# Kernel optimization log

Hardware: AMD Instinct MI355X
Metric: run time of the kernel (lower is better)

Reference implementation:

```python
import jax, jax.numpy as jnp
import numpy as np
import math

H = 5       # attention heads
DK = 20     # attdim // H
ATT = 100   # attdim
LAYERS = 2
B, L, BERT_DIM = 32, 256, 768


def _layernorm(x, a, b, eps=1e-6):
    mean = x.mean(-1, keepdims=True)
    std = jnp.std(x, axis=-1, ddof=1, keepdims=True)  # torch.std is unbiased
    return a * (x - mean) / (std + eps) + b


def _forward(sequence_output, src_mask, aspect_mask, short_mask,
             ln_a, ln_b, Wxx_w, Wxx_b, q_w, q_b, k_w, k_b,
             dense_w, dense_b, bias_m, W_w, W_b, Wx_w, Wx_b, clf_w, clf_b):
    Bn, Ln, _ = sequence_output.shape
    x = _layernorm(sequence_output, ln_a, ln_b)
    g = x @ Wxx_w + Wxx_b                                  # [B,L,100]
    asp_wn = aspect_mask.sum(1, keepdims=True)             # [B,1]
    aspect = (g * aspect_mask[..., None]).sum(1) / asp_wn  # [B,100]

    q = (g @ q_w + q_b).reshape(Bn, Ln, H, DK).transpose(0, 2, 1, 3)  # [B,H,L,dk]
    k = (g @ k_w + k_b).reshape(Bn, Ln, H, DK).transpose(0, 2, 1, 3)
    # aspect is expanded identically across heads/positions before dense -> [B,dk]
    asp = aspect @ dense_w + dense_b                       # [B,dk]
    scores = jnp.einsum('bhid,bhjd->bhij', q, k) / math.sqrt(DK)
    asp_sc = jnp.tanh(jnp.einsum('bd,bhjd->bhj', asp, k) + bias_m[0])
    scores = scores + asp_sc[:, :, None, :]
    scores = jnp.where(src_mask[:, None, None, :] == 0, -1e9, scores)
    scores = scores + short_mask                           # [B,1,L,L] broadcast
    adj = jax.nn.softmax(scores, axis=-1)                  # [B,H,L,L]

    # edge-update linear split so the [B,L,L,205] concat is never materialized:
    # edge[b,i,j] = adj_perm[b,i,j] @ Wa + go[b,j] @ W1 + go[b,i] @ W2 + b
    Wa, W1, W2 = Wx_w[:H], Wx_w[H:H + ATT], Wx_w[H + ATT:]
    go = g
    for i in range(LAYERS):
        # expand+matmul+mean over heads == mean-head message passing
        Ax = jnp.einsum('bhij,bjd->bid', adj, go) / H
        go = jax.nn.relu(Ax @ W_w + W_b)
        if i < LAYERS - 1:  # last edge update is discarded by the original output
            edge = (jnp.einsum('bhij,hk->bijk', adj, Wa)
                    + (go @ W1)[:, None, :, :]
                    + (go @ W2)[:, :, None, :]
                    + Wx_b)
            adj = edge.transpose(0, 3, 1, 2)
    # original: node_outputs = F.relu(gcn_outputs) (aggregate_W result is overwritten)
    h = jax.nn.relu(go)
    out1 = (h * aspect_mask[..., None]).sum(1) / asp_wn    # [B,100]
    return out1 @ clf_w + clf_b                            # [B,3]


def setup_inputs() -> dict:
    key = jax.random.key(0)
    ks = jax.random.split(key, 24)
    f32 = jnp.float32
    p = lambda k, shape, s=0.05: jax.random.normal(k, shape, dtype=f32) * s
    src_mask = jax.random.randint(ks[0], (B, L), 0, 2, dtype=jnp.int32).at[:, 0].set(1)
    aspect_mask = jnp.zeros((B, L), f32).at[:, 4:8].set(1.0)  # aspect span tokens
    return {
        'sequence_output': jax.random.normal(ks[1], (B, L, BERT_DIM), dtype=f32),
        'src_mask': src_mask,
        'aspect_mask': aspect_mask,
        'short_mask': p(ks[2], (B, 1, L, L), 1.0),
        'ln_a': jnp.ones((BERT_DIM,), f32),
        'ln_b': jnp.zeros((BERT_DIM,), f32),
        'Wxx_w': p(ks[3], (BERT_DIM, ATT)), 'Wxx_b': p(ks[4], (ATT,)),
        'q_w': p(ks[5], (ATT, ATT)), 'q_b': p(ks[6], (ATT,)),
        'k_w': p(ks[7], (ATT, ATT)), 'k_b': p(ks[8], (ATT,)),
        'dense_w': p(ks[9], (ATT, DK)), 'dense_b': p(ks[10], (DK,)),
        'bias_m': p(ks[11], (1,)),
        'W_w': p(ks[12], (ATT, ATT)), 'W_b': p(ks[13], (ATT,)),
        'Wx_w': p(ks[14], (H + 2 * ATT, H)), 'Wx_b': p(ks[15], (H,)),
        'clf_w': p(ks[16], (ATT, 3)), 'clf_b': p(ks[17], (3,)),
    }


def reference(sequence_output, src_mask, aspect_mask, short_mask,
              ln_a, ln_b, Wxx_w, Wxx_b, q_w, q_b, k_w, k_b,
              dense_w, dense_b, bias_m, W_w, W_b, Wx_w, Wx_b, clf_w, clf_b):
    return _forward(sequence_output, src_mask, aspect_mask, short_mask,
                    ln_a, ln_b, Wxx_w, Wxx_b, q_w, q_b, k_w, k_b,
                    dense_w, dense_b, bias_m, W_w, W_b, Wx_w, Wx_b, clf_w, clf_b)
```

## Files before the change

kernel.cpp:

```cpp
#include <hip/hip_runtime.h>
#include <math.h>

constexpr int CL = 256;
constexpr int CD = 768;
constexpr int CATT = 100;
constexpr int CH = 5;
constexpr int CDK = 20;

__device__ __forceinline__ void fma4(float4& a, float s, const float4& w) {
    a.x = fmaf(s, w.x, a.x);
    a.y = fmaf(s, w.y, a.y);
    a.z = fmaf(s, w.z, a.z);
    a.w = fmaf(s, w.w, a.w);
}

__global__ __launch_bounds__(256, 3) void k1_fused(
    const float* __restrict__ x, const float* __restrict__ ln_a,
    const float* __restrict__ ln_b, const float* __restrict__ Wxx_w,
    const float* __restrict__ Wxx_b, const float* __restrict__ q_w,
    const float* __restrict__ q_b, const float* __restrict__ k_w,
    const float* __restrict__ k_b, const float* __restrict__ amask,
    float* __restrict__ g, float* __restrict__ qt, float* __restrict__ ktb,
    float* __restrict__ aspect_raw)
{
    __shared__ float s_w[2][3200];
    __shared__ float s_xn[2][16 * 36];
    __shared__ float s_gt[16 * 100];
    __shared__ float s_ln[1536];
    __shared__ float s_mean[16], s_rinv[16];

    const int t = threadIdx.x;
    const int r0 = blockIdx.x * 16;
    const int wid = t >> 6, lane = t & 63;

    if (t < 192) {
        ((float4*)s_ln)[t] = ((const float4*)ln_a)[t];
        ((float4*)(s_ln + 768))[t] = ((const float4*)ln_b)[t];
    }

    for (int rr = wid * 4; rr < wid * 4 + 4; ++rr) {
        const float* xr = x + (size_t)(r0 + rr) * CD;
        float xv[12];
        float s = 0.f;
#pragma unroll
        for (int m = 0; m < 12; ++m) { xv[m] = xr[lane + 64 * m]; s += xv[m]; }
#pragma unroll
        for (int o = 32; o; o >>= 1) s += __shfl_xor(s, o);
        float mean = s * (1.0f / 768.0f);
        float sq = 0.f;
#pragma unroll
        for (int m = 0; m < 12; ++m) { float d = xv[m] - mean; sq = fmaf(d, d, sq); }
#pragma unroll
        for (int o = 32; o; o >>= 1) sq += __shfl_xor(sq, o);
        if (lane == 0) {
            s_mean[rr] = mean;
            s_rinv[rr] = 1.0f / (sqrtf(sq * (1.0f / 767.0f)) + 1e-6f);
        }
    }

    const float4* wsrc = (const float4*)Wxx_w;
    float4 w0 = wsrc[t], w1 = wsrc[t + 256], w2 = wsrc[t + 512], w3;
    if (t < 32) w3 = wsrc[t + 768];
    const int rA = t >> 5, cA = t & 31;
    float xa = x[(size_t)(r0 + rA) * CD + cA];
    float xb = x[(size_t)(r0 + rA + 8) * CD + cA];

    __syncthreads();

    {
        float4* d4 = (float4*)s_w[0];
        d4[t] = w0; d4[t + 256] = w1; d4[t + 512] = w2;
        if (t < 32) d4[t + 768] = w3;
        float la = s_ln[cA], lbv = s_ln[768 + cA];
        s_xn[0][rA * 36 + cA] = fmaf(la, (xa - s_mean[rA]) * s_rinv[rA], lbv);
        s_xn[0][(rA + 8) * 36 + cA] = fmaf(la, (xb - s_mean[rA + 8]) * s_rinv[rA + 8], lbv);
    }
    __syncthreads();

    const int cg = t % 25, rg = t / 25;
    const int c = cg * 4;
    float4 acc0 = make_float4(0.f, 0.f, 0.f, 0.f);
    float4 acc1 = make_float4(0.f, 0.f, 0.f, 0.f);

    for (int kt = 0; kt < 24; ++kt) {
        if (kt < 23) {
            const float4* ws = wsrc + (size_t)(kt + 1) * 800;
            w0 = ws[t]; w1 = ws[t + 256]; w2 = ws[t + 512];
            if (t < 32) w3 = ws[t + 768];
            int gc = (kt + 1) * 32 + cA;
            xa = x[(size_t)(r0 + rA) * CD + gc];
            xb = x[(size_t)(r0 + rA + 8) * CD + gc];
        }
        if (t < 200) {
            const float* wb = s_w[kt & 1];
            const float* xbuf = s_xn[kt & 1];
#pragma unroll 2
            for (int kk = 0; kk < 32; kk += 4) {
                float4 a0 = *(const float4*)&xbuf[(rg * 2 + 0) * 36 + kk];
                float4 a1 = *(const float4*)&xbuf[(rg * 2 + 1) * 36 + kk];
                float4 v0 = *(const float4*)&wb[(kk + 0) * 100 + c];
                float4 v1 = *(const float4*)&wb[(kk + 1) * 100 + c];
                float4 v2 = *(const float4*)&wb[(kk + 2) * 100 + c];
                float4 v3 = *(const float4*)&wb[(kk + 3) * 100 + c];
                fma4(acc0, a0.x, v0); fma4(acc0, a0.y, v1); fma4(acc0, a0.z, v2); fma4(acc0, a0.w, v3);
                fma4(acc1, a1.x, v0); fma4(acc1, a1.y, v1); fma4(acc1, a1.z, v2); fma4(acc1, a1.w, v3);
            }
        }
        if (kt < 23) {
            float4* d4 = (float4*)s_w[(kt + 1) & 1];
            d4[t] = w0; d4[t + 256] = w1; d4[t + 512] = w2;
            if (t < 32) d4[t + 768] = w3;
            int gc = (kt + 1) * 32 + cA;
            float la = s_ln[gc], lbv = s_ln[768 + gc];
            float* xd = s_xn[(kt + 1) & 1];
            xd[rA * 36 + cA] = fmaf(la, (xa - s_mean[rA]) * s_rinv[rA], lbv);
            xd[(rA + 8) * 36 + cA] = fmaf(la, (xb - s_mean[rA + 8]) * s_rinv[rA + 8], lbv);
        }
        __syncthreads();
    }

    if (t < 200) {
        float4 bias = *(const float4*)&Wxx_b[c];
        float4 rv0, rv1;
        rv0.x = acc0.x + bias.x; rv0.y = acc0.y + bias.y; rv0.z = acc0.z + bias.z; rv0.w = acc0.w + bias.w;
        rv1.x = acc1.x + bias.x; rv1.y = acc1.y + bias.y; rv1.z = acc1.z + bias.z; rv1.w = acc1.w + bias.w;
        float4 rv[2] = { rv0, rv1 };
#pragma unroll
        for (int q = 0; q < 2; ++q) {
            int row = r0 + rg * 2 + q;
            *(float4*)&g[(size_t)row * CATT + c] = rv[q];
            *(float4*)&s_gt[(rg * 2 + q) * 100 + c] = rv[q];
            float m = amask[row];
            if (m != 0.f) {
                int b = row >> 8;
                atomicAdd(&aspect_raw[b * CATT + c + 0], m * rv[q].x);
                atomicAdd(&aspect_raw[b * CATT + c + 1], m * rv[q].y);
                atomicAdd(&aspect_raw[b * CATT + c + 2], m * rv[q].z);
                atomicAdd(&aspect_raw[b * CATT + c + 3], m * rv[q].w);
            }
        }
    }

    const float4* qw4 = (const float4*)q_w;
    const float4* kw4 = (const float4*)k_w;
    float4 sA = qw4[t], sB;
    if (t < 244) sB = qw4[t + 256];
    __syncthreads();
    {
        float4* d4 = (float4*)s_w[0];
        d4[t] = sA; if (t < 244) d4[t + 256] = sB;
    }
    __syncthreads();

    float4 p0 = make_float4(0.f, 0.f, 0.f, 0.f);
    float4 p1 = make_float4(0.f, 0.f, 0.f, 0.f);
    for (int tau = 0; tau < 10; ++tau) {
        if (tau < 9) {
            const float4* src = (tau + 1 < 5) ? qw4 + (size_t)(tau + 1) * 500
                                              : kw4 + (size_t)(tau - 4) * 500;
            sA = src[t]; if (t < 244) sB = src[t + 256];
        }
        if (t < 200) {
            const float* wb = s_w[tau & 1];
            const int kb = (tau % 5) * 20;
#pragma unroll 2
            for (int kk = 0; kk < 20; kk += 4) {
                float4 a0 = *(const float4*)&s_gt[(rg * 2 + 0) * 100 + kb + kk];
                float4 a1 = *(const float4*)&s_gt[(rg * 2 + 1) * 100 + kb + kk];
                float4 v0 = *(const float4*)&wb[(kk + 0) * 100 + c];
                float4 v1 = *(const float4*)&wb[(kk + 1) * 100 + c];
                float4 v2 = *(const float4*)&wb[(kk + 2) * 100 + c];
                float4 v3 = *(const float4*)&wb[(kk + 3) * 100 + c];
                fma4(p0, a0.x, v0); fma4(p0, a0.y, v1); fma4(p0, a0.z, v2); fma4(p0, a0.w, v3);
                fma4(p1, a1.x, v0); fma4(p1, a1.y, v1); fma4(p1, a1.z, v2); fma4(p1, a1.w, v3);
            }
            if (tau == 4 || tau == 9) {
                const float* bb = (tau == 4) ? q_b : k_b;
                float* outp = (tau == 4) ? qt : ktb;
                float4 bias = *(const float4*)&bb[c];
                p0.x += bias.x; p0.y += bias.y; p0.z += bias.z; p0.w += bias.w;
                p1.x += bias.x; p1.y += bias.y; p1.z += bias.z; p1.w += bias.w;
                const int h = c / CDK, d = c % CDK;
                float4 rv[2] = { p0, p1 };
#pragma unroll
                for (int q = 0; q < 2; ++q) {
                    int row = r0 + rg * 2 + q;
                    int bidx = row >> 8, l = row & 255;
                    *(float4*)&outp[((size_t)(bidx * CH + h) * CL + l) * CDK + d] = rv[q];
                }
                p0 = make_float4(0.f, 0.f, 0.f, 0.f);
                p1 = make_float4(0.f, 0.f, 0.f, 0.f);
            }
        }
        if (tau < 9) {
            float4* d4 = (float4*)s_w[(tau + 1) & 1];
            d4[t] = sA; if (t < 244) d4[t + 256] = sB;
        }
        __syncthreads();
    }
}

__global__ __launch_bounds__(256, 3) void k45_attn_gcn0(
    const float* __restrict__ qt, const float* __restrict__ ktb,
    const float* __restrict__ aspect_raw, const float* __restrict__ amask,
    const float* __restrict__ dense_w, const float* __restrict__ dense_b,
    const float* __restrict__ bias_m, const int* __restrict__ src_mask,
    const float* __restrict__ shortm, const float* __restrict__ Wx_w,
    const float* __restrict__ g, const float* __restrict__ W_w,
    const float* __restrict__ W_b, float* __restrict__ adjW,
    float* __restrict__ go1, float* __restrict__ t1, float* __restrict__ t2,
    float* __restrict__ gW2S)
{
    constexpr int ICH = 16;
    __shared__ float s_pool[16 * 260];
    __shared__ float s_w[2][3200];
    __shared__ float s_q[CH * 320];
    __shared__ float s_red[CH][64];
    __shared__ float s_was[5];
    __shared__ float s_aspb[20];
    __shared__ float s_w1[100], s_w2[100];
    __shared__ float s_g1row[16];

    const int b = blockIdx.x >> 4, ic = blockIdx.x & 15;
    const int i0 = ic * ICH;
    const int t = threadIdx.x, lane = t & 63, wid = t >> 6;
    const int j = t;

    if (t < 5) {
        float s = 0.f;
        for (int k2 = 0; k2 < 5; ++k2) s += Wx_w[t * 5 + k2];
        s_was[t] = s;
    }
    if (t < 100) {
        float a = 0.f, c2 = 0.f;
#pragma unroll
        for (int h = 0; h < 5; ++h) {
            a += Wx_w[(5 + t) * 5 + h];
            c2 += Wx_w[(105 + t) * 5 + h];
        }
        s_w1[t] = a; s_w2[t] = c2;
    }
    float wn = 0.f;
    if (t < 64) {
        float4 mv = ((const float4*)amask)[b * 64 + t];
        wn = mv.x + mv.y + mv.z + mv.w;
#pragma unroll
        for (int o = 32; o; o >>= 1) wn += __shfl_xor(wn, o);
    }
    if (t < 20) {
        float a = 0.f;
        for (int d = 0; d < CATT; ++d)
            a = fmaf(aspect_raw[b * CATT + d], dense_w[d * CDK + t], a);
        s_aspb[t] = a / wn + dense_b[t];
    }
    {
        const float* qbase = qt + (size_t)b * CH * CL * CDK + (size_t)i0 * CDK;
        for (int i = t; i < CH * 320; i += 256) {
            int h = i / 320, r = i % 320;
            s_q[i] = qbase[(size_t)h * CL * CDK + r];
        }
    }

    const bool masked = (src_mask[b * CL + j] == 0);
    const float bm = bias_m[0];
    const float rs20 = 0.223606797749978969f;

    float sm[ICH];
#pragma unroll
    for (int ii = 0; ii < ICH; ++ii)
        sm[ii] = shortm[(size_t)(b * CL + i0 + ii) * CL + j];

    float accS[ICH], accW[ICH];
#pragma unroll
    for (int ii = 0; ii < ICH; ++ii) { accS[ii] = 0.f; accW[ii] = 0.f; }

    __syncthreads();

    for (int h = 0; h < CH; ++h) {
        float4 kr[5];
        const float* kp = ktb + ((size_t)(b * CH + h) * CL + j) * CDK;
#pragma unroll
        for (int m = 0; m < 5; ++m) kr[m] = *(const float4*)(kp + 4 * m);
        const float was_h = s_was[h];
        float s = bm;
#pragma unroll
        for (int m = 0; m < 5; ++m) {
            s = fmaf(s_aspb[4 * m + 0], kr[m].x, s);
            s = fmaf(s_aspb[4 * m + 1], kr[m].y, s);
            s = fmaf(s_aspb[4 * m + 2], kr[m].z, s);
            s = fmaf(s_aspb[4 * m + 3], kr[m].w, s);
        }
        const float aspsc = tanhf(s);

        float pv[ICH];
#pragma unroll
        for (int ii = 0; ii < ICH; ++ii) {
            const float* qrow = &s_q[h * 320 + ii * CDK];
            float sc = 0.f;
#pragma unroll
            for (int m = 0; m < 5; ++m) {
                float4 q4 = *(const float4*)(qrow + 4 * m);
                sc = fmaf(q4.x, kr[m].x, sc);
                sc = fmaf(q4.y, kr[m].y, sc);
                sc = fmaf(q4.z, kr[m].z, sc);
                sc = fmaf(q4.w, kr[m].w, sc);
            }
            sc = fmaf(sc, rs20, aspsc) + sm[ii];
            float p = masked ? 0.f : __expf(sc);
            pv[ii] = p;
            float ssum = p;
#pragma unroll
            for (int o = 32; o; o >>= 1) ssum += __shfl_xor(ssum, o);
            if (lane == 0) s_red[h][ii * 4 + wid] = ssum;
        }
        __syncthreads();
#pragma unroll
        for (int ii = 0; ii < ICH; ++ii) {
            float tot = s_red[h][ii * 4 + 0] + s_red[h][ii * 4 + 1] +
                        s_red[h][ii * 4 + 2] + s_red[h][ii * 4 + 3];
            float pn = pv[ii] * __frcp_rn(tot);
            accS[ii] += pn;
            accW[ii] = fmaf(was_h, pn, accW[ii]);
        }
    }

#pragma unroll
    for (int ii = 0; ii < ICH; ++ii) {
        adjW[(size_t)(b * CL + i0 + ii) * CL + j] = accW[ii];
        s_pool[ii * 260 + j] = accS[ii];
    }

    const int cg = t % 25, rg = t / 25;
    const int c = cg * 4;
    const float4* g4 = (const float4*)g + (size_t)b * 6400;
    float4 sA = g4[t], sB = g4[t + 256], sC = g4[t + 512], sD;
    if (t < 32) sD = g4[t + 768];
    {
        float4* d4 = (float4*)s_w[0];
        d4[t] = sA; d4[t + 256] = sB; d4[t + 512] = sC;
        if (t < 32) d4[t + 768] = sD;
    }
    __syncthreads();

    float4 acc0 = make_float4(0.f, 0.f, 0.f, 0.f);
    float4 acc1 = make_float4(0.f, 0.f, 0.f, 0.f);
    for (int jt = 0; jt < 8; ++jt) {
        if (jt < 7) {
            const float4* src = g4 + (size_t)(jt + 1) * 800;
            sA = src[t]; sB = src[t + 256]; sC = src[t + 512];
            if (t < 32) sD = src[t + 768];
        }
        if (t < 200) {
            const float* wb = s_w[jt & 1];
#pragma unroll 2
            for (int kk = 0; kk < 32; kk += 4) {
                float4 a0 = *(const float4*)&s_pool[(rg * 2 + 0) * 260 + jt * 32 + kk];
                float4 a1 = *(const float4*)&s_pool[(rg * 2 + 1) * 260 + jt * 32 + kk];
                float4 v0 = *(const float4*)&wb[(kk + 0) * 100 + c];
                float4 v1 = *(const float4*)&wb[(kk + 1) * 100 + c];
                float4 v2 = *(const float4*)&wb[(kk + 2) * 100 + c];
                float4 v3 = *(const float4*)&wb[(kk + 3) * 100 + c];
                fma4(acc0, a0.x, v0); fma4(acc0, a0.y, v1); fma4(acc0, a0.z, v2); fma4(acc0, a0.w, v3);
                fma4(acc1, a1.x, v0); fma4(acc1, a1.y, v1); fma4(acc1, a1.z, v2); fma4(acc1, a1.w, v3);
            }
        }
        if (jt < 7) {
            float4* d4 = (float4*)s_w[(jt + 1) & 1];
            d4[t] = sA; d4[t + 256] = sB; d4[t + 512] = sC;
            if (t < 32) d4[t + 768] = sD;
        }
        __syncthreads();
    }

    float* s_ax = s_pool;
    if (t < 200) {
        float4 r;
        r.x = acc0.x * 0.2f; r.y = acc0.y * 0.2f; r.z = acc0.z * 0.2f; r.w = acc0.w * 0.2f;
        *(float4*)&s_ax[(rg * 2 + 0) * 108 + c] = r;
        r.x = acc1.x * 0.2f; r.y = acc1.y * 0.2f; r.z = acc1.z * 0.2f; r.w = acc1.w * 0.2f;
        *(float4*)&s_ax[(rg * 2 + 1) * 108 + c] = r;
    }
    const float4* ww4 = (const float4*)W_w;
    sA = ww4[t]; if (t < 244) sB = ww4[t + 256];
    {
        float4* d4 = (float4*)s_w[0];
        d4[t] = sA; if (t < 244) d4[t + 256] = sB;
    }
    __syncthreads();

    float4 o0 = make_float4(0.f, 0.f, 0.f, 0.f);
    float4 o1 = make_float4(0.f, 0.f, 0.f, 0.f);
    for (int wt = 0; wt < 5; ++wt) {
        if (wt < 4) {
            const float4* src = ww4 + (size_t)(wt + 1) * 500;
            sA = src[t]; if (t < 244) sB = src[t + 256];
        }
        if (t < 200) {
            const float* wb = s_w[wt & 1];
            const int kb = wt * 20;
#pragma unroll 2
            for (int kk = 0; kk < 20; kk += 4) {
                float4 a0 = *(const float4*)&s_ax[(rg * 2 + 0) * 108 + kb + kk];
                float4 a1 = *(const float4*)&s_ax[(rg * 2 + 1) * 108 + kb + kk];
                float4 v0 = *(const float4*)&wb[(kk + 0) * 100 + c];
                float4 v1 = *(const float4*)&wb[(kk + 1) * 100 + c];
                float4 v2 = *(const float4*)&wb[(kk + 2) * 100 + c];
                float4 v3 = *(const float4*)&wb[(kk + 3) * 100 + c];
                fma4(o0, a0.x, v0); fma4(o0, a0.y, v1); fma4(o0, a0.z, v2); fma4(o0, a0.w, v3);
                fma4(o1, a1.x, v0); fma4(o1, a1.y, v1); fma4(o1, a1.z, v2); fma4(o1, a1.w, v3);
            }
        }
        if (wt < 4) {
            float4* d4 = (float4*)s_w[(wt + 1) & 1];
            d4[t] = sA; if (t < 244) d4[t + 256] = sB;
        }
        __syncthreads();
    }

    float* s_go = s_pool + 1728;
    if (t < 200) {
        float4 bias = *(const float4*)&W_b[c];
        o0.x = fmaxf(o0.x + bias.x, 0.f); o0.y = fmaxf(o0.y + bias.y, 0.f);
        o0.z = fmaxf(o0.z + bias.z, 0.f); o0.w = fmaxf(o0.w + bias.w, 0.f);
        o1.x = fmaxf(o1.x + bias.x, 0.f); o1.y = fmaxf(o1.y + bias.y, 0.f);
        o1.z = fmaxf(o1.z + bias.z, 0.f); o1.w = fmaxf(o1.w + bias.w, 0.f);
        *(float4*)&go1[(size_t)(b * CL + i0 + rg * 2 + 0) * CATT + c] = o0;
        *(float4*)&go1[(size_t)(b * CL + i0 + rg * 2 + 1) * CATT + c] = o1;
        *(float4*)&s_go[(rg * 2 + 0) * 104 + c] = o0;
        *(float4*)&s_go[(rg * 2 + 1) * 104 + c] = o1;
    }
    __syncthreads();

    if (t < 128) {
        int r = t >> 3, seg = t & 7;
        int e0 = seg * 13, e1 = e0 + 13 < 100 ? e0 + 13 : 100;
        float a = 0.f, c2 = 0.f;
        for (int e = e0; e < e1; ++e) {
            float v = s_go[r * 104 + e];
            a = fmaf(v, s_w1[e], a);
            c2 = fmaf(v, s_w2[e], c2);
        }
        a += __shfl_xor(a, 1); a += __shfl_xor(a, 2); a += __shfl_xor(a, 4);
        c2 += __shfl_xor(c2, 1); c2 += __shfl_xor(c2, 2); c2 += __shfl_xor(c2, 4);
        if (seg == 0) {
            s_g1row[r] = a;
            gW2S[b * CL + i0 + r] = c2;
        }
    }
    __syncthreads();

    if (t < 100) {
        float a = 0.f, s2 = 0.f;
#pragma unroll
        for (int r = 0; r < 16; ++r) {
            float v = s_go[r * 104 + t];
            a = fmaf(s_g1row[r], v, a);
            s2 += v;
        }
        atomicAdd(&t1[b * CATT + t], a);
        atomicAdd(&t2[b * CATT + t], s2);
    }
}

__global__ __launch_bounds__(256, 3) void k7_gcn1(
    const float* __restrict__ adjW, const float* __restrict__ go1,
    const float* __restrict__ W_w, const float* __restrict__ W_b,
    const float* __restrict__ t1, const float* __restrict__ t2,
    const float* __restrict__ gW2S, const float* __restrict__ Wx_b,
    const float* __restrict__ amask, float* __restrict__ out1_raw)
{
    __shared__ float s_pool[16 * 260];
    __shared__ float s_w[2][3200];
    const int b = blockIdx.x >> 4, ic = blockIdx.x & 15;
    const int i0 = ic * 16;
    const int t = threadIdx.x;

    {
        const float4* asrc = (const float4*)adjW + (size_t)(b * CL + i0) * 64;
#pragma unroll
        for (int m = 0; m < 4; ++m) {
            int i = t + 256 * m;
            int row = i >> 6, c4 = i & 63;
            *(float4*)&s_pool[row * 260 + c4 * 4] = asrc[i];
        }
    }
    const int cg = t % 25, rg = t / 25;
    const int c = cg * 4;
    const float4* g4 = (const float4*)go1 + (size_t)b * 6400;
    float4 sA = g4[t], sB = g4[t + 256], sC = g4[t + 512], sD;
    if (t < 32) sD = g4[t + 768];
    {
        float4* d4 = (float4*)s_w[0];
        d4[t] = sA; d4[t + 256] = sB; d4[t + 512] = sC;
        if (t < 32) d4[t + 768] = sD;
    }
    __syncthreads();

    float4 acc0 = make_float4(0.f, 0.f, 0.f, 0.f);
    float4 acc1 = make_float4(0.f, 0.f, 0.f, 0.f);
    for (int jt = 0; jt < 8; ++jt) {
        if (jt < 7) {
            const float4* src = g4 + (size_t)(jt + 1) * 800;
            sA = src[t]; sB = src[t + 256]; sC = src[t + 512];
            if (t < 32) sD = src[t + 768];
        }
        if (t < 200) {
            const float* wb = s_w[jt & 1];
#pragma unroll 2
            for (int kk = 0; kk < 32; kk += 4) {
                float4 a0 = *(const float4*)&s_pool[(rg * 2 + 0) * 260 + jt * 32 + kk];
                float4 a1 = *(const float4*)&s_pool[(rg * 2 + 1) * 260 + jt * 32 + kk];
                float4 v0 = *(const float4*)&wb[(kk + 0) * 100 + c];
                float4 v1 = *(const float4*)&wb[(kk + 1) * 100 + c];
                float4 v2 = *(const float4*)&wb[(kk + 2) * 100 + c];
                float4 v3 = *(const float4*)&wb[(kk + 3) * 100 + c];
                fma4(acc0, a0.x, v0); fma4(acc0, a0.y, v1); fma4(acc0, a0.z, v2); fma4(acc0, a0.w, v3);
                fma4(acc1, a1.x, v0); fma4(acc1, a1.y, v1); fma4(acc1, a1.z, v2); fma4(acc1, a1.w, v3);
            }
        }
        if (jt < 7) {
            float4* d4 = (float4*)s_w[(jt + 1) & 1];
            d4[t] = sA; d4[t + 256] = sB; d4[t + 512] = sC;
            if (t < 32) d4[t + 768] = sD;
        }
        __syncthreads();
    }

    float* s_ax = s_pool;
    if (t < 200) {
        float wxbs = Wx_b[0] + Wx_b[1] + Wx_b[2] + Wx_b[3] + Wx_b[4];
        float4 t1v = *(const float4*)&t1[b * CATT + c];
        float4 t2v = *(const float4*)&t2[b * CATT + c];
        float gw0 = gW2S[b * CL + i0 + rg * 2 + 0] + wxbs;
        float gw1 = gW2S[b * CL + i0 + rg * 2 + 1] + wxbs;
        float4 r;
        r.x = (acc0.x + t1v.x + gw0 * t2v.x) * 0.2f;
        r.y = (acc0.y + t1v.y + gw0 * t2v.y) * 0.2f;
        r.z = (acc0.z + t1v.z + gw0 * t2v.z) * 0.2f;
        r.w = (acc0.w + t1v.w + gw0 * t2v.w) * 0.2f;
        *(float4*)&s_ax[(rg * 2 + 0) * 108 + c] = r;
        r.x = (acc1.x + t1v.x + gw1 * t2v.x) * 0.2f;
        r.y = (acc1.y + t1v.y + gw1 * t2v.y) * 0.2f;
        r.z = (acc1.z + t1v.z + gw1 * t2v.z) * 0.2f;
        r.w = (acc1.w + t1v.w + gw1 * t2v.w) * 0.2f;
        *(float4*)&s_ax[(rg * 2 + 1) * 108 + c] = r;
    }
    const float4* ww4 = (const float4*)W_w;
    sA = ww4[t]; if (t < 244) sB = ww4[t + 256];
    {
        float4* d4 = (float4*)s_w[0];
        d4[t] = sA; if (t < 244) d4[t + 256] = sB;
    }
    __syncthreads();

    float4 o0 = make_float4(0.f, 0.f, 0.f, 0.f);
    float4 o1 = make_float4(0.f, 0.f, 0.f, 0.f);
    for (int wt = 0; wt < 5; ++wt) {
        if (wt < 4) {
            const float4* src = ww4 + (size_t)(wt + 1) * 500;
            sA = src[t]; if (t < 244) sB = src[t + 256];
        }
        if (t < 200) {
            const float* wb = s_w[wt & 1];
            const int kb = wt * 20;
#pragma unroll 2
            for (int kk = 0; kk < 20; kk += 4) {
                float4 a0 = *(const float4*)&s_ax[(rg * 2 + 0) * 108 + kb + kk];
                float4 a1 = *(const float4*)&s_ax[(rg * 2 + 1) * 108 + kb + kk];
                float4 v0 = *(const float4*)&wb[(kk + 0) * 100 + c];
                float4 v1 = *(const float4*)&wb[(kk + 1) * 100 + c];
                float4 v2 = *(const float4*)&wb[(kk + 2) * 100 + c];
                float4 v3 = *(const float4*)&wb[(kk + 3) * 100 + c];
                fma4(o0, a0.x, v0); fma4(o0, a0.y, v1); fma4(o0, a0.z, v2); fma4(o0, a0.w, v3);
                fma4(o1, a1.x, v0); fma4(o1, a1.y, v1); fma4(o1, a1.z, v2); fma4(o1, a1.w, v3);
            }
        }
        if (wt < 4) {
            float4* d4 = (float4*)s_w[(wt + 1) & 1];
            d4[t] = sA; if (t < 244) d4[t + 256] = sB;
        }
        __syncthreads();
    }

    if (t < 200) {
        float4 bias = *(const float4*)&W_b[c];
        o0.x = fmaxf(o0.x + bias.x, 0.f); o0.y = fmaxf(o0.y + bias.y, 0.f);
        o0.z = fmaxf(o0.z + bias.z, 0.f); o0.w = fmaxf(o0.w + bias.w, 0.f);
        o1.x = fmaxf(o1.x + bias.x, 0.f); o1.y = fmaxf(o1.y + bias.y, 0.f);
        o1.z = fmaxf(o1.z + bias.z, 0.f); o1.w = fmaxf(o1.w + bias.w, 0.f);
        float4 ov[2] = { o0, o1 };
#pragma unroll
        for (int q = 0; q < 2; ++q) {
            int row = b * CL + i0 + rg * 2 + q;
            float m = amask[row];
            if (m != 0.f) {
                atomicAdd(&out1_raw[b * CATT + c + 0], m * ov[q].x);
                atomicAdd(&out1_raw[b * CATT + c + 1], m * ov[q].y);
                atomicAdd(&out1_raw[b * CATT + c + 2], m * ov[q].z);
                atomicAdd(&out1_raw[b * CATT + c + 3], m * ov[q].w);
            }
        }
    }
}

__global__ __launch_bounds__(64) void k8_small(
    const float* __restrict__ out1_raw, const float* __restrict__ amask,
    const float* __restrict__ clf_w, const float* __restrict__ clf_b,
    float* __restrict__ out)
{
    const int b = blockIdx.x, t = threadIdx.x;
    float4 mv = ((const float4*)amask)[b * 64 + t];
    float wn = mv.x + mv.y + mv.z + mv.w;
#pragma unroll
    for (int o = 32; o; o >>= 1) wn += __shfl_xor(wn, o);
    if (t < 3) {
        float rwn = 1.f / wn;
        float a = clf_b[t];
        for (int d = 0; d < CATT; ++d)
            a = fmaf(out1_raw[b * CATT + d] * rwn, clf_w[d * 3 + t], a);
        out[b * 3 + t] = a;
    }
}

extern "C" void kernel_launch(void* const* d_in, const int* in_sizes, int n_in,
                              void* d_out, int out_size, void* d_ws, size_t ws_size,
                              hipStream_t stream) {
    const float* seq     = (const float*)d_in[0];
    const int*   srcm    = (const int*)d_in[1];
    const float* amask   = (const float*)d_in[2];
    const float* shortm  = (const float*)d_in[3];
    const float* ln_a    = (const float*)d_in[4];
    const float* ln_b    = (const float*)d_in[5];
    const float* Wxx_w   = (const float*)d_in[6];
    const float* Wxx_b   = (const float*)d_in[7];
    const float* q_w     = (const float*)d_in[8];
    const float* q_b     = (const float*)d_in[9];
    const float* k_w     = (const float*)d_in[10];
    const float* k_b     = (const float*)d_in[11];
    const float* dense_w = (const float*)d_in[12];
    const float* dense_b = (const float*)d_in[13];
    const float* bias_m  = (const float*)d_in[14];
    const float* W_w     = (const float*)d_in[15];
    const float* W_b     = (const float*)d_in[16];
    const float* Wx_w    = (const float*)d_in[17];
    const float* Wx_b    = (const float*)d_in[18];
    const float* clf_w   = (const float*)d_in[19];
    const float* clf_b   = (const float*)d_in[20];
    float* out = (float*)d_out;

    float* ws         = (float*)d_ws;
    float* g          = ws;
    float* qt         = g + 819200;
    float* ktb        = qt + 819200;
    float* go1        = ktb + 819200;
    float* adjW       = go1 + 819200;
    float* aspect_raw = adjW + 2097152;
    float* t1         = aspect_raw + 3200;
    float* t2         = t1 + 3200;
    float* out1_raw   = t2 + 3200;
    float* gW2S       = out1_raw + 3200;

    hipMemsetAsync(aspect_raw, 0, 4 * 3200 * sizeof(float), stream);
    hipLaunchKernelGGL(k1_fused, dim3(512), dim3(256), 0, stream, seq, ln_a, ln_b,
                       Wxx_w, Wxx_b, q_w, q_b, k_w, k_b, amask, g, qt, ktb, aspect_raw);
    hipLaunchKernelGGL(k45_attn_gcn0, dim3(512), dim3(256), 0, stream,
                       qt, ktb, aspect_raw, amask, dense_w, dense_b, bias_m, srcm,
                       shortm, Wx_w, g, W_w, W_b, adjW, go1, t1, t2, gW2S);
    hipLaunchKernelGGL(k7_gcn1, dim3(512), dim3(256), 0, stream,
                       adjW, go1, W_w, W_b, t1, t2, gW2S, Wx_b, amask, out1_raw);
    hipLaunchKernelGGL(k8_small, dim3(32), dim3(64), 0, stream,
                       out1_raw, amask, clf_w, clf_b, out);
}
```

Before: 241.8 us.

## Fuse all stages into one cooperative persistent kernel with grid syncs

Merges the three main kernels and the classifier into a single cooperative kernel that uses grid-wide syncs between phases, with a fallback to separate launches if cooperative launch is unavailable. Each block keeps its adjW tile in shared memory across the phase boundary, so the global adjW write and re-read are dropped. This removes launch gaps and adjW traffic. In exchange, the larger shared-memory struct lowers occupancy to 2 blocks per CU, grid syncs add barrier cost, and an occupancy query runs on the host at every launch.

```diff
diff --git a/kernel.cpp b/kernel.cpp
--- a/kernel.cpp
+++ b/kernel.cpp
@@ -1,5 +1,8 @@
 #include <hip/hip_runtime.h>
+#include <hip/hip_cooperative_groups.h>
 #include <math.h>
+
+namespace cg = cooperative_groups;
 
 constexpr int CL = 256;
 constexpr int CD = 768;
@@ -14,7 +17,19 @@
     a.w = fmaf(s, w.w, a.w);
 }
 
-__global__ __launch_bounds__(256, 3) void k1_fused(
+struct SMem {
+    float w[2][3200];
+    float adjW[4160];
+    float pool[4160];
+    float q[1600];
+    float red[5][64];
+    float was[5], aspb[20];
+    float w1[100], w2[100], g1row[16];
+    float mean[16], rinv[16];
+};
+
+__device__ __forceinline__ void phase0(
+    SMem& sm, int blk, int t,
     const float* __restrict__ x, const float* __restrict__ ln_a,
     const float* __restrict__ ln_b, const float* __restrict__ Wxx_w,
     const float* __restrict__ Wxx_b, const float* __restrict__ q_w,
@@ -23,21 +38,17 @@
     float* __restrict__ g, float* __restrict__ qt, float* __restrict__ ktb,
     float* __restrict__ aspect_raw)
 {
-    __shared__ float s_w[2][3200];
-    __shared__ float s_xn[2][16 * 36];
-    __shared__ float s_gt[16 * 100];
-    __shared__ float s_ln[1536];
-    __shared__ float s_mean[16], s_rinv[16];
-
-    const int t = threadIdx.x;
-    const int r0 = blockIdx.x * 16;
+    const int r0 = blk * 16;
     const int wid = t >> 6, lane = t & 63;
+    float* s_gt = sm.pool;
+    float* s_ln = sm.pool + 1600;
+    float* s_xn0 = sm.q;
+    float* s_xn1 = sm.q + 576;
 
     if (t < 192) {
         ((float4*)s_ln)[t] = ((const float4*)ln_a)[t];
         ((float4*)(s_ln + 768))[t] = ((const float4*)ln_b)[t];
     }
-
     for (int rr = wid * 4; rr < wid * 4 + 4; ++rr) {
         const float* xr = x + (size_t)(r0 + rr) * CD;
         float xv[12];
@@ -53,8 +64,8 @@
 #pragma unroll
         for (int o = 32; o; o >>= 1) sq += __shfl_xor(sq, o);
         if (lane == 0) {
-            s_mean[rr] = mean;
-            s_rinv[rr] = 1.0f / (sqrtf(sq * (1.0f / 767.0f)) + 1e-6f);
+            sm.mean[rr] = mean;
+            sm.rinv[rr] = 1.0f / (sqrtf(sq * (1.0f / 767.0f)) + 1e-6f);
         }
     }
 
@@ -68,17 +79,17 @@
     __syncthreads();
 
     {
-        float4* d4 = (float4*)s_w[0];
+        float4* d4 = (float4*)sm.w[0];
         d4[t] = w0; d4[t + 256] = w1; d4[t + 512] = w2;
         if (t < 32) d4[t + 768] = w3;
         float la = s_ln[cA], lbv = s_ln[768 + cA];
-        s_xn[0][rA * 36 + cA] = fmaf(la, (xa - s_mean[rA]) * s_rinv[rA], lbv);
-        s_xn[0][(rA + 8) * 36 + cA] = fmaf(la, (xb - s_mean[rA + 8]) * s_rinv[rA + 8], lbv);
-    }
-    __syncthreads();
-
-    const int cg = t % 25, rg = t / 25;
-    const int c = cg * 4;
+        s_xn0[rA * 36 + cA] = fmaf(la, (xa - sm.mean[rA]) * sm.rinv[rA], lbv);
+        s_xn0[(rA + 8) * 36 + cA] = fmaf(la, (xb - sm.mean[rA + 8]) * sm.rinv[rA + 8], lbv);
+    }
+    __syncthreads();
+
+    const int cg2 = t % 25, rg = t / 25;
+    const int c = cg2 * 4;
     float4 acc0 = make_float4(0.f, 0.f, 0.f, 0.f);
     float4 acc1 = make_float4(0.f, 0.f, 0.f, 0.f);
 
@@ -92,8 +103,8 @@
             xb = x[(size_t)(r0 + rA + 8) * CD + gc];
         }
         if (t < 200) {
-            const float* wb = s_w[kt & 1];
-            const float* xbuf = s_xn[kt & 1];
+            const float* wb = sm.w[kt & 1];
+            const float* xbuf = (kt & 1) ? s_xn1 : s_xn0;
 #pragma unroll 2
             for (int kk = 0; kk < 32; kk += 4) {
                 float4 a0 = *(const float4*)&xbuf[(rg * 2 + 0) * 36 + kk];
@@ -107,14 +118,14 @@
             }
         }
         if (kt < 23) {
-            float4* d4 = (float4*)s_w[(kt + 1) & 1];
+            float4* d4 = (float4*)sm.w[(kt + 1) & 1];
             d4[t] = w0; d4[t + 256] = w1; d4[t + 512] = w2;
             if (t < 32) d4[t + 768] = w3;
             int gc = (kt + 1) * 32 + cA;
             float la = s_ln[gc], lbv = s_ln[768 + gc];
-            float* xd = s_xn[(kt + 1) & 1];
-            xd[rA * 36 + cA] = fmaf(la, (xa - s_mean[rA]) * s_rinv[rA], lbv);
-            xd[(rA + 8) * 36 + cA] = fmaf(la, (xb - s_mean[rA + 8]) * s_rinv[rA + 8], lbv);
+            float* xd = ((kt + 1) & 1) ? s_xn1 : s_xn0;
+            xd[rA * 36 + cA] = fmaf(la, (xa - sm.mean[rA]) * sm.rinv[rA], lbv);
+            xd[(rA + 8) * 36 + cA] = fmaf(la, (xb - sm.mean[rA + 8]) * sm.rinv[rA + 8], lbv);
         }
         __syncthreads();
     }
@@ -147,7 +158,7 @@
     if (t < 244) sB = qw4[t + 256];
     __syncthreads();
     {
-        float4* d4 = (float4*)s_w[0];
+        float4* d4 = (float4*)sm.w[0];
         d4[t] = sA; if (t < 244) d4[t + 256] = sB;
     }
     __syncthreads();
@@ -161,7 +172,7 @@
             sA = src[t]; if (t < 244) sB = src[t + 256];
         }
         if (t < 200) {
-            const float* wb = s_w[tau & 1];
+            const float* wb = sm.w[tau & 1];
             const int kb = (tau % 5) * 20;
 #pragma unroll 2
             for (int kk = 0; kk < 20; kk += 4) {
@@ -193,43 +204,35 @@
             }
         }
         if (tau < 9) {
-            float4* d4 = (float4*)s_w[(tau + 1) & 1];
+            float4* d4 = (float4*)sm.w[(tau + 1) & 1];
             d4[t] = sA; if (t < 244) d4[t + 256] = sB;
         }
         __syncthreads();
     }
 }
 
-__global__ __launch_bounds__(256, 3) void k45_attn_gcn0(
+__device__ __forceinline__ void phase1(
+    SMem& sm, int blk, int t,
     const float* __restrict__ qt, const float* __restrict__ ktb,
     const float* __restrict__ aspect_raw, const float* __restrict__ amask,
     const float* __restrict__ dense_w, const float* __restrict__ dense_b,
     const float* __restrict__ bias_m, const int* __restrict__ src_mask,
     const float* __restrict__ shortm, const float* __restrict__ Wx_w,
     const float* __restrict__ g, const float* __restrict__ W_w,
-    const float* __restrict__ W_b, float* __restrict__ adjW,
-    float* __restrict__ go1, float* __restrict__ t1, float* __restrict__ t2,
-    float* __restrict__ gW2S)
+    const float* __restrict__ W_b, float* __restrict__ go1,
+    float* __restrict__ t1, float* __restrict__ t2, float* __restrict__ gW2S,
+    float* __restrict__ adjW_global)
 {
     constexpr int ICH = 16;
-    __shared__ float s_pool[16 * 260];
-    __shared__ float s_w[2][3200];
-    __shared__ float s_q[CH * 320];
-    __shared__ float s_red[CH][64];
-    __shared__ float s_was[5];
-    __shared__ float s_aspb[20];
-    __shared__ float s_w1[100], s_w2[100];
-    __shared__ float s_g1row[16];
-
-    const int b = blockIdx.x >> 4, ic = blockIdx.x & 15;
+    const int b = blk >> 4, ic = blk & 15;
     const int i0 = ic * ICH;
-    const int t = threadIdx.x, lane = t & 63, wid = t >> 6;
+    const int lane = t & 63, wid = t >> 6;
     const int j = t;
 
     if (t < 5) {
         float s = 0.f;
         for (int k2 = 0; k2 < 5; ++k2) s += Wx_w[t * 5 + k2];
-        s_was[t] = s;
+        sm.was[t] = s;
     }
     if (t < 100) {
         float a = 0.f, c2 = 0.f;
@@ -238,7 +241,7 @@
             a += Wx_w[(5 + t) * 5 + h];
             c2 += Wx_w[(105 + t) * 5 + h];
         }
-        s_w1[t] = a; s_w2[t] = c2;
+        sm.w1[t] = a; sm.w2[t] = c2;
     }
     float wn = 0.f;
     if (t < 64) {
@@ -251,13 +254,13 @@
         float a = 0.f;
         for (int d = 0; d < CATT; ++d)
             a = fmaf(aspect_raw[b * CATT + d], dense_w[d * CDK + t], a);
-        s_aspb[t] = a / wn + dense_b[t];
+        sm.aspb[t] = a / wn + dense_b[t];
     }
     {
         const float* qbase = qt + (size_t)b * CH * CL * CDK + (size_t)i0 * CDK;
         for (int i = t; i < CH * 320; i += 256) {
             int h = i / 320, r = i % 320;
-            s_q[i] = qbase[(size_t)h * CL * CDK + r];
+            sm.q[i] = qbase[(size_t)h * CL * CDK + r];
         }
     }
 
@@ -265,10 +268,10 @@
     const float bm = bias_m[0];
     const float rs20 = 0.223606797749978969f;
 
-    float sm[ICH];
+    float smv[ICH];
 #pragma unroll
     for (int ii = 0; ii < ICH; ++ii)
-        sm[ii] = shortm[(size_t)(b * CL + i0 + ii) * CL + j];
+        smv[ii] = shortm[(size_t)(b * CL + i0 + ii) * CL + j];
 
     float accS[ICH], accW[ICH];
 #pragma unroll
@@ -281,21 +284,21 @@
         const float* kp = ktb + ((size_t)(b * CH + h) * CL + j) * CDK;
 #pragma unroll
         for (int m = 0; m < 5; ++m) kr[m] = *(const float4*)(kp + 4 * m);
-        const float was_h = s_was[h];
+        const float was_h = sm.was[h];
         float s = bm;
 #pragma unroll
         for (int m = 0; m < 5; ++m) {
-            s = fmaf(s_aspb[4 * m + 0], kr[m].x, s);
-            s = fmaf(s_aspb[4 * m + 1], kr[m].y, s);
-            s = fmaf(s_aspb[4 * m + 2], kr[m].z, s);
-            s = fmaf(s_aspb[4 * m + 3], kr[m].w, s);
+            s = fmaf(sm.aspb[4 * m + 0], kr[m].x, s);
+            s = fmaf(sm.aspb[4 * m + 1], kr[m].y, s);
+            s = fmaf(sm.aspb[4 * m + 2], kr[m].z, s);
+            s = fmaf(sm.aspb[4 * m + 3], kr[m].w, s);
         }
         const float aspsc = tanhf(s);
 
         float pv[ICH];
 #pragma unroll
         for (int ii = 0; ii < ICH; ++ii) {
-            const float* qrow = &s_q[h * 320 + ii * CDK];
+            const float* qrow = &sm.q[h * 320 + ii * CDK];
             float sc = 0.f;
 #pragma unroll
             for (int m = 0; m < 5; ++m) {
@@ -305,19 +308,19 @@
                 sc = fmaf(q4.z, kr[m].z, sc);
                 sc = fmaf(q4.w, kr[m].w, sc);
             }
-            sc = fmaf(sc, rs20, aspsc) + sm[ii];
+            sc = fmaf(sc, rs20, aspsc) + smv[ii];
             float p = masked ? 0.f : __expf(sc);
             pv[ii] = p;
             float ssum = p;
 #pragma unroll
             for (int o = 32; o; o >>= 1) ssum += __shfl_xor(ssum, o);
-            if (lane == 0) s_red[h][ii * 4 + wid] = ssum;
+            if (lane == 0) sm.red[h][ii * 4 + wid] = ssum;
         }
         __syncthreads();
 #pragma unroll
         for (int ii = 0; ii < ICH; ++ii) {
-            float tot = s_red[h][ii * 4 + 0] + s_red[h][ii * 4 + 1] +
-                        s_red[h][ii * 4 + 2] + s_red[h][ii * 4 + 3];
+            float tot = sm.red[h][ii * 4 + 0] + sm.red[h][ii * 4 + 1] +
+                        sm.red[h][ii * 4 + 2] + sm.red[h][ii * 4 + 3];
             float pn = pv[ii] * __frcp_rn(tot);
             accS[ii] += pn;
             accW[ii] = fmaf(was_h, pn, accW[ii]);
@@ -326,17 +329,22 @@
 
 #pragma unroll
     for (int ii = 0; ii < ICH; ++ii) {
-        adjW[(size_t)(b * CL + i0 + ii) * CL + j] = accW[ii];
-        s_pool[ii * 260 + j] = accS[ii];
-    }
-
-    const int cg = t % 25, rg = t / 25;
-    const int c = cg * 4;
+        sm.adjW[ii * 260 + j] = accW[ii];
+        sm.pool[ii * 260 + j] = accS[ii];
+    }
+    if (adjW_global) {
+#pragma unroll
+        for (int ii = 0; ii < ICH; ++ii)
+            adjW_global[(size_t)(b * CL + i0 + ii) * CL + j] = accW[ii];
+    }
+
+    const int cg2 = t % 25, rg = t / 25;
+    const int c = cg2 * 4;
     const float4* g4 = (const float4*)g + (size_t)b * 6400;
     float4 sA = g4[t], sB = g4[t + 256], sC = g4[t + 512], sD;
     if (t < 32) sD = g4[t + 768];
     {
-        float4* d4 = (float4*)s_w[0];
+        float4* d4 = (float4*)sm.w[0];
         d4[t] = sA; d4[t + 256] = sB; d4[t + 512] = sC;
         if (t < 32) d4[t + 768] = sD;
     }
@@ -351,11 +359,11 @@
             if (t < 32) sD = src[t + 768];
         }
         if (t < 200) {
-            const float* wb = s_w[jt & 1];
+            const float* wb = sm.w[jt & 1];
 #pragma unroll 2
             for (int kk = 0; kk < 32; kk += 4) {
-                float4 a0 = *(const float4*)&s_pool[(rg * 2 + 0) * 260 + jt * 32 + kk];
-                float4 a1 = *(const float4*)&s_pool[(rg * 2 + 1) * 260 + jt * 32 + kk];
+                float4 a0 = *(const float4*)&sm.pool[(rg * 2 + 0) * 260 + jt * 32 + kk];
+                float4 a1 = *(const float4*)&sm.pool[(rg * 2 + 1) * 260 + jt * 32 + kk];
                 float4 v0 = *(const float4*)&wb[(kk + 0) * 100 + c];
                 float4 v1 = *(const float4*)&wb[(kk + 1) * 100 + c];
                 float4 v2 = *(const float4*)&wb[(kk + 2) * 100 + c];
@@ -365,14 +373,14 @@
             }
         }
         if (jt < 7) {
-            float4* d4 = (float4*)s_w[(jt + 1) & 1];
+            float4* d4 = (float4*)sm.w[(jt + 1) & 1];
             d4[t] = sA; d4[t + 256] = sB; d4[t + 512] = sC;
             if (t < 32) d4[t + 768] = sD;
         }
         __syncthreads();
     }
 
-    float* s_ax = s_pool;
+    float* s_ax = sm.pool;
     if (t < 200) {
         float4 r;
         r.x = acc0.x * 0.2f; r.y = acc0.y * 0.2f; r.z = acc0.z * 0.2f; r.w = acc0.w * 0.2f;
@@ -383,7 +391,7 @@
     const float4* ww4 = (const float4*)W_w;
     sA = ww4[t]; if (t < 244) sB = ww4[t + 256];
     {
-        float4* d4 = (float4*)s_w[0];
+        float4* d4 = (float4*)sm.w[0];
         d4[t] = sA; if (t < 244) d4[t + 256] = sB;
     }
     __syncthreads();
@@ -396,7 +404,7 @@
             sA = src[t]; if (t < 244) sB = src[t + 256];
         }
         if (t < 200) {
-            const float* wb = s_w[wt & 1];
+            const float* wb = sm.w[wt & 1];
             const int kb = wt * 20;
 #pragma unroll 2
             for (int kk = 0; kk < 20; kk += 4) {
@@ -411,13 +419,13 @@
             }
         }
         if (wt < 4) {
-            float4* d4 = (float4*)s_w[(wt + 1) & 1];
+            float4* d4 = (float4*)sm.w[(wt + 1) & 1];
             d4[t] = sA; if (t < 244) d4[t + 256] = sB;
         }
         __syncthreads();
     }
 
-    float* s_go = s_pool + 1728;
+    float* s_go = sm.pool + 1728;
     if (t < 200) {
         float4 bias = *(const float4*)&W_b[c];
         o0.x = fmaxf(o0.x + bias.x, 0.f); o0.y = fmaxf(o0.y + bias.y, 0.f);
@@ -437,13 +445,13 @@
         float a = 0.f, c2 = 0.f;
         for (int e = e0; e < e1; ++e) {
             float v = s_go[r * 104 + e];
-            a = fmaf(v, s_w1[e], a);
-            c2 = fmaf(v, s_w2[e], c2);
+            a = fmaf(v, sm.w1[e], a);
+            c2 = fmaf(v, sm.w2[e], c2);
         }
         a += __shfl_xor(a, 1); a += __shfl_xor(a, 2); a += __shfl_xor(a, 4);
         c2 += __shfl_xor(c2, 1); c2 += __shfl_xor(c2, 2); c2 += __shfl_xor(c2, 4);
         if (seg == 0) {
-            s_g1row[r] = a;
+            sm.g1row[r] = a;
             gW2S[b * CL + i0 + r] = c2;
         }
     }
@@ -454,7 +462,7 @@
 #pragma unroll
         for (int r = 0; r < 16; ++r) {
             float v = s_go[r * 104 + t];
-            a = fmaf(s_g1row[r], v, a);
+            a = fmaf(sm.g1row[r], v, a);
             s2 += v;
         }
         atomicAdd(&t1[b * CATT + t], a);
@@ -462,35 +470,24 @@
     }
 }
 
-__global__ __launch_bounds__(256, 3) void k7_gcn1(
-    const float* __restrict__ adjW, const float* __restrict__ go1,
-    const float* __restrict__ W_w, const float* __restrict__ W_b,
-    const float* __restrict__ t1, const float* __restrict__ t2,
-    const float* __restrict__ gW2S, const float* __restrict__ Wx_b,
-    const float* __restrict__ amask, float* __restrict__ out1_raw)
-{
-    __shared__ float s_pool[16 * 260];
-    __shared__ float s_w[2][3200];
-    const int b = blockIdx.x >> 4, ic = blockIdx.x & 15;
+__device__ __forceinline__ void phase2(
+    SMem& sm, int blk, int t,
+    const float* __restrict__ go1, const float* __restrict__ W_w,
+    const float* __restrict__ W_b, const float* __restrict__ t1,
+    const float* __restrict__ t2, const float* __restrict__ gW2S,
+    const float* __restrict__ Wx_b, const float* __restrict__ amask,
+    float* __restrict__ out1_raw)
+{
+    const int b = blk >> 4, ic = blk & 15;
     const int i0 = ic * 16;
-    const int t = threadIdx.x;
-
-    {
-        const float4* asrc = (const float4*)adjW + (size_t)(b * CL + i0) * 64;
-#pragma unroll
-        for (int m = 0; m < 4; ++m) {
-            int i = t + 256 * m;
-            int row = i >> 6, c4 = i & 63;
-            *(float4*)&s_pool[row * 260 + c4 * 4] = asrc[i];
-        }
-    }
-    const int cg = t % 25, rg = t / 25;
-    const int c = cg * 4;
+    const int cg2 = t % 25, rg = t / 25;
+    const int c = cg2 * 4;
+
     const float4* g4 = (const float4*)go1 + (size_t)b * 6400;
     float4 sA = g4[t], sB = g4[t + 256], sC = g4[t + 512], sD;
     if (t < 32) sD = g4[t + 768];
     {
-        float4* d4 = (float4*)s_w[0];
+        float4* d4 = (float4*)sm.w[0];
         d4[t] = sA; d4[t + 256] = sB; d4[t + 512] = sC;
         if (t < 32) d4[t + 768] = sD;
     }
@@ -505,11 +502,11 @@
             if (t < 32) sD = src[t + 768];
         }
         if (t < 200) {
-            const float* wb = s_w[jt & 1];
+            const float* wb = sm.w[jt & 1];
 #pragma unroll 2
             for (int kk = 0; kk < 32; kk += 4) {
-                float4 a0 = *(const float4*)&s_pool[(rg * 2 + 0) * 260 + jt * 32 + kk];
-                float4 a1 = *(const float4*)&s_pool[(rg * 2 + 1) * 260 + jt * 32 + kk];
+                float4 a0 = *(const float4*)&sm.adjW[(rg * 2 + 0) * 260 + jt * 32 + kk];
+                float4 a1 = *(const float4*)&sm.adjW[(rg * 2 + 1) * 260 + jt * 32 + kk];
                 float4 v0 = *(const float4*)&wb[(kk + 0) * 100 + c];
                 float4 v1 = *(const float4*)&wb[(kk + 1) * 100 + c];
                 float4 v2 = *(const float4*)&wb[(kk + 2) * 100 + c];
@@ -519,14 +516,14 @@
             }
         }
         if (jt < 7) {
-            float4* d4 = (float4*)s_w[(jt + 1) & 1];
+            float4* d4 = (float4*)sm.w[(jt + 1) & 1];
             d4[t] = sA; d4[t + 256] = sB; d4[t + 512] = sC;
             if (t < 32) d4[t + 768] = sD;
         }
         __syncthreads();
     }
 
-    float* s_ax = s_pool;
+    float* s_ax = sm.pool;
     if (t < 200) {
         float wxbs = Wx_b[0] + Wx_b[1] + Wx_b[2] + Wx_b[3] + Wx_b[4];
         float4 t1v = *(const float4*)&t1[b * CATT + c];
@@ -548,7 +545,7 @@
     const float4* ww4 = (const float4*)W_w;
     sA = ww4[t]; if (t < 244) sB = ww4[t + 256];
     {
-        float4* d4 = (float4*)s_w[0];
+        float4* d4 = (float4*)sm.w[0];
         d4[t] = sA; if (t < 244) d4[t + 256] = sB;
     }
     __syncthreads();
@@ -561,7 +558,7 @@
             sA = src[t]; if (t < 244) sB = src[t + 256];
         }
         if (t < 200) {
-            const float* wb = s_w[wt & 1];
+            const float* wb = sm.w[wt & 1];
             const int kb = wt * 20;
 #pragma unroll 2
             for (int kk = 0; kk < 20; kk += 4) {
@@ -576,7 +573,7 @@
             }
         }
         if (wt < 4) {
-            float4* d4 = (float4*)s_w[(wt + 1) & 1];
+            float4* d4 = (float4*)sm.w[(wt + 1) & 1];
             d4[t] = sA; if (t < 244) d4[t + 256] = sB;
         }
         __syncthreads();
@@ -603,23 +600,106 @@
     }
 }
 
-__global__ __launch_bounds__(64) void k8_small(
-    const float* __restrict__ out1_raw, const float* __restrict__ amask,
-    const float* __restrict__ clf_w, const float* __restrict__ clf_b,
-    float* __restrict__ out)
-{
-    const int b = blockIdx.x, t = threadIdx.x;
-    float4 mv = ((const float4*)amask)[b * 64 + t];
-    float wn = mv.x + mv.y + mv.z + mv.w;
-#pragma unroll
-    for (int o = 32; o; o >>= 1) wn += __shfl_xor(wn, o);
-    if (t < 3) {
-        float rwn = 1.f / wn;
-        float a = clf_b[t];
-        for (int d = 0; d < CATT; ++d)
-            a = fmaf(out1_raw[b * CATT + d] * rwn, clf_w[d * 3 + t], a);
-        out[b * 3 + t] = a;
-    }
+__device__ __forceinline__ void phase3(
+    int blk, int t, const float* __restrict__ out1_raw,
+    const float* __restrict__ amask, const float* __restrict__ clf_w,
+    const float* __restrict__ clf_b, float* __restrict__ out)
+{
+    if (blk < 32 && t < 64) {
+        const int b = blk;
+        float4 mv = ((const float4*)amask)[b * 64 + t];
+        float wn = mv.x + mv.y + mv.z + mv.w;
+#pragma unroll
+        for (int o = 32; o; o >>= 1) wn += __shfl_xor(wn, o);
+        if (t < 3) {
+            float rwn = 1.f / wn;
+            float a = clf_b[t];
+            for (int d = 0; d < CATT; ++d)
+                a = fmaf(out1_raw[b * CATT + d] * rwn, clf_w[d * 3 + t], a);
+            out[b * 3 + t] = a;
+        }
+    }
+}
+
+__global__ __launch_bounds__(256, 2) void k_all(
+    const float* x, const float* ln_a, const float* ln_b, const float* Wxx_w,
+    const float* Wxx_b, const float* q_w, const float* q_b, const float* k_w,
+    const float* k_b, const float* amask, const int* src_mask,
+    const float* shortm, const float* dense_w, const float* dense_b,
+    const float* bias_m, const float* Wx_w, const float* Wx_b,
+    const float* W_w, const float* W_b, const float* clf_w,
+    const float* clf_b, float* g, float* qt, float* ktb, float* go1,
+    float* aspect_raw, float* t1, float* t2, float* out1_raw, float* gW2S,
+    float* out)
+{
+    __shared__ SMem sm;
+    const int t = threadIdx.x, blk = blockIdx.x;
+    cg::grid_group grid = cg::this_grid();
+
+    phase0(sm, blk, t, x, ln_a, ln_b, Wxx_w, Wxx_b, q_w, q_b, k_w, k_b,
+           amask, g, qt, ktb, aspect_raw);
+    __threadfence();
+    grid.sync();
+    phase1(sm, blk, t, qt, ktb, aspect_raw, amask, dense_w, dense_b, bias_m,
+           src_mask, shortm, Wx_w, g, W_w, W_b, go1, t1, t2, gW2S, nullptr);
+    __threadfence();
+    grid.sync();
+    phase2(sm, blk, t, go1, W_w, W_b, t1, t2, gW2S, Wx_b, amask, out1_raw);
+    __threadfence();
+    grid.sync();
+    phase3(blk, t, out1_raw, amask, clf_w, clf_b, out);
+}
+
+__global__ __launch_bounds__(256, 2) void kP0(
+    const float* x, const float* ln_a, const float* ln_b, const float* Wxx_w,
+    const float* Wxx_b, const float* q_w, const float* q_b, const float* k_w,
+    const float* k_b, const float* amask, float* g, float* qt, float* ktb,
+    float* aspect_raw)
+{
+    __shared__ SMem sm;
+    phase0(sm, blockIdx.x, threadIdx.x, x, ln_a, ln_b, Wxx_w, Wxx_b,
+           q_w, q_b, k_w, k_b, amask, g, qt, ktb, aspect_raw);
+}
+
+__global__ __launch_bounds__(256, 2) void kP1(
+    const float* qt, const float* ktb, const float* aspect_raw,
+    const float* amask, const float* dense_w, const float* dense_b,
+    const float* bias_m, const int* src_mask, const float* shortm,
+    const float* Wx_w, const float* g, const float* W_w, const float* W_b,
+    float* go1, float* t1, float* t2, float* gW2S, float* adjW)
+{
+    __shared__ SMem sm;
+    phase1(sm, blockIdx.x, threadIdx.x, qt, ktb, aspect_raw, amask, dense_w,
+           dense_b, bias_m, src_mask, shortm, Wx_w, g, W_w, W_b, go1,
+           t1, t2, gW2S, adjW);
+}
+
+__global__ __launch_bounds__(256, 2) void kP2(
+    const float* adjW, const float* go1, const float* W_w, const float* W_b,
+    const float* t1, const float* t2, const float* gW2S, const float* Wx_b,
+    const float* amask, float* out1_raw)
+{
+    __shared__ SMem sm;
+    const int t = threadIdx.x;
+    const int b = blockIdx.x >> 4, ic = blockIdx.x & 15;
+    {
+        const float4* asrc = (const float4*)adjW + (size_t)(b * CL + ic * 16) * 64;
+#pragma unroll
+        for (int m = 0; m < 4; ++m) {
+            int i = t + 256 * m;
+            int row = i >> 6, c4 = i & 63;
+            *(float4*)&sm.adjW[row * 260 + c4 * 4] = asrc[i];
+        }
+    }
+    __syncthreads();
+    phase2(sm, blockIdx.x, t, go1, W_w, W_b, t1, t2, gW2S, Wx_b, amask, out1_raw);
+}
+
+__global__ __launch_bounds__(64) void kP3(
+    const float* out1_raw, const float* amask, const float* clf_w,
+    const float* clf_b, float* out)
+{
+    phase3(blockIdx.x, threadIdx.x, out1_raw, amask, clf_w, clf_b, out);
 }
 
 extern "C" void kernel_launch(void* const* d_in, const int* in_sizes, int n_in,
@@ -661,13 +741,35 @@
     float* gW2S       = out1_raw + 3200;
 
     hipMemsetAsync(aspect_raw, 0, 4 * 3200 * sizeof(float), stream);
-    hipLaunchKernelGGL(k1_fused, dim3(512), dim3(256), 0, stream, seq, ln_a, ln_b,
-                       Wxx_w, Wxx_b, q_w, q_b, k_w, k_b, amask, g, qt, ktb, aspect_raw);
-    hipLaunchKernelGGL(k45_attn_gcn0, dim3(512), dim3(256), 0, stream,
-                       qt, ktb, aspect_raw, amask, dense_w, dense_b, bias_m, srcm,
-                       shortm, Wx_w, g, W_w, W_b, adjW, go1, t1, t2, gW2S);
-    hipLaunchKernelGGL(k7_gcn1, dim3(512), dim3(256), 0, stream,
-                       adjW, go1, W_w, W_b, t1, t2, gW2S, Wx_b, amask, out1_raw);
-    hipLaunchKernelGGL(k8_small, dim3(32), dim3(64), 0, stream,
-                       out1_raw, amask, clf_w, clf_b, out);
-}
+
+    int maxb = 0;
+    hipError_t qerr = hipOccupancyMaxActiveBlocksPerMultiprocessor(
+        &maxb, reinterpret_cast<const void*>(k_all), 256, 0);
+    bool coop = (qerr == hipSuccess && maxb >= 2);
+
+    if (coop) {
+        void* args[] = {
+            (void*)&seq, (void*)&ln_a, (void*)&ln_b, (void*)&Wxx_w, (void*)&Wxx_b,
+            (void*)&q_w, (void*)&q_b, (void*)&k_w, (void*)&k_b, (void*)&amask,
+            (void*)&srcm, (void*)&shortm, (void*)&dense_w, (void*)&dense_b,
+            (void*)&bias_m, (void*)&Wx_w, (void*)&Wx_b, (void*)&W_w, (void*)&W_b,
+            (void*)&clf_w, (void*)&clf_b, (void*)&g, (void*)&qt, (void*)&ktb,
+            (void*)&go1, (void*)&aspect_raw, (void*)&t1, (void*)&t2,
+            (void*)&out1_raw, (void*)&gW2S, (void*)&out
+        };
+        hipError_t lerr = hipLaunchCooperativeKernel(
+            (void*)k_all, dim3(512), dim3(256), args, 0, stream);
+        if (lerr != hipSuccess) { (void)hipGetLastError(); coop = false; }
+    }
+    if (!coop) {
+        hipLaunchKernelGGL(kP0, dim3(512), dim3(256), 0, stream, seq, ln_a, ln_b,
+                           Wxx_w, Wxx_b, q_w, q_b, k_w, k_b, amask, g, qt, ktb, aspect_raw);
+        hipLaunchKernelGGL(kP1, dim3(512), dim3(256), 0, stream, qt, ktb, aspect_raw,
+                           amask, dense_w, dense_b, bias_m, srcm, shortm, Wx_w,
+                           g, W_w, W_b, go1, t1, t2, gW2S, adjW);
+        hipLaunchKernelGGL(kP2, dim3(512), dim3(256), 0, stream, adjW, go1, W_w, W_b,
+                           t1, t2, gW2S, Wx_b, amask, out1_raw);
+        hipLaunchKernelGGL(kP3, dim3(32), dim3(64), 0, stream, out1_raw, amask,
+                           clf_w, clf_b, out);
+    }
+}
```

Result: slower. 246.7 us (+2.1%).
